# Kernel optimization log

Measured on AMD Instinct MI355X. Metric: run time of the kernel, lower is better.

## Reference

```python
import jax, jax.numpy as jnp
import numpy as np

B, S, H, A, F, NCATE, VOCAB, EMB, NCONT = 64, 1024, 512, 256, 2048, 4, 1000, 64, 4


def _layernorm(x, g, b, eps=1e-5):
    m = jnp.mean(x, axis=-1, keepdims=True)
    v = jnp.mean((x - m) ** 2, axis=-1, keepdims=True)
    return (x - m) * jax.lax.rsqrt(v + eps) * g + b


def _positional_encoding(seq_len, d, base=10000.0):
    pos = jnp.arange(seq_len, dtype=jnp.float32)[:, None]
    i = jnp.arange(0, d, 2, dtype=jnp.float32)[None, :]
    ang = pos / jnp.power(base, i / d)
    pe = jnp.zeros((seq_len, d), dtype=jnp.float32)
    pe = pe.at[:, 0::2].set(jnp.sin(ang))
    pe = pe.at[:, 1::2].set(jnp.cos(ang))
    return pe


def setup_inputs() -> dict:
    key = jax.random.key(0)
    ks = jax.random.split(key, 24)
    s = lambda i, shape, fan: jax.random.normal(ks[i], shape, jnp.float32) / np.sqrt(fan)
    inp = {
        'cate_x': jax.random.randint(ks[0], (B, S, NCATE), 0, VOCAB, jnp.int32),
        'cont_x': jax.random.normal(ks[1], (B, S, NCONT), jnp.float32),
        'mask': (jax.random.uniform(ks[2], (B, S)) < 0.9).astype(jnp.float32),
        'targets': jax.random.uniform(ks[3], (B, S), jnp.float32),
        'E_cate': s(4, (NCATE, VOCAB, EMB), EMB),
        'W_proj': s(5, (NCATE * EMB + NCONT, H), NCATE * EMB + NCONT),
        'WQ1': s(6, (H, A), H), 'WK1': s(7, (H, A), H), 'WV1': s(8, (H, A), H),
        'WQ2': s(9, (H, A), H), 'WK2': s(10, (H, A), H), 'WV2': s(11, (H, A), H),
        'W0': s(12, (2 * A, H), 2 * A),
        'ln1_g': jnp.ones((H,), jnp.float32), 'ln1_b': jnp.zeros((H,), jnp.float32),
        'Wf1': s(13, (H, F), H), 'bf1': jnp.zeros((F,), jnp.float32),
        'Wf2': s(14, (F, H), F), 'bf2': jnp.zeros((H,), jnp.float32),
        'ln2_g': jnp.ones((H,), jnp.float32), 'ln2_b': jnp.zeros((H,), jnp.float32),
        'Wfin': s(15, (H, 1), H), 'bfin': jnp.zeros((1,), jnp.float32),
    }
    return inp


def _attn_branch(x, WQ, WK, WV, mask_bias):
    Q = x @ WQ  # [B,S,A]
    K = x @ WK
    V = x @ WV
    scores = jnp.einsum('bsa,bta->bst', Q, K) / np.sqrt(A)
    scores = scores + mask_bias  # additive key-mask [B,1,S]
    return jnp.einsum('bst,bta->bsa', jax.nn.softmax(scores, axis=-1), V)


def reference(cate_x, cont_x, mask, targets, E_cate, W_proj, WQ1, WK1, WV1,
              WQ2, WK2, WV2, W0, ln1_g, ln1_b, Wf1, bf1, Wf2, bf2, ln2_g,
              ln2_b, Wfin, bfin):
    # embedding: per-feature lookup, concat with continuous, project to hidden
    emb = jax.vmap(lambda tab, idx: tab[idx], in_axes=(0, 2), out_axes=2)(E_cate, cate_x)
    emb = emb.reshape(B, S, NCATE * EMB)
    x = jnp.concatenate([emb, cont_x], axis=-1) @ W_proj  # [B,S,H]
    x = x + _positional_encoding(S, H)[None]
    mask_bias = (mask * 1e6 - 1e6)[:, None, :]  # [B,1,S]
    z1 = _attn_branch(x, WQ1, WK1, WV1, mask_bias)
    z2 = _attn_branch(x, WQ2, WK2, WV2, mask_bias)
    z = jnp.concatenate([z1, z2], axis=-1) @ W0
    z = _layernorm(x + z, ln1_g, ln1_b)
    fz = jax.nn.relu(z @ Wf1 + bf1) @ Wf2 + bf2
    z3 = _layernorm(z + fz, ln2_g, ln2_b)
    out = (z3 @ Wfin + bfin).squeeze(-1)  # [B,S]
    return out
```

## Files before the change

### kernel.cpp

```cpp
#include <hip/hip_runtime.h>

typedef unsigned short ushort_t;
typedef unsigned int uint32;
typedef float f32x4 __attribute__((ext_vector_type(4)));
typedef short bf16x8 __attribute__((ext_vector_type(8)));

__device__ __forceinline__ float bf2f(short u) {
  union { uint32 u32; float f; } cv;
  cv.u32 = ((uint32)(ushort_t)u) << 16;
  return cv.f;
}
__device__ __forceinline__ ushort_t f2bf(float f) {
  union { float f; uint32 u; } cv; cv.f = f;
  return (ushort_t)((cv.u + 0x7fffu + ((cv.u >> 16) & 1u)) >> 16);
}
__device__ __forceinline__ uint32 pack2bf(float lo, float hi) {
  return (uint32)f2bf(lo) | ((uint32)f2bf(hi) << 16);
}
__device__ __forceinline__ f32x4 mfma16(bf16x8 a, bf16x8 b, f32x4 c) {
  return __builtin_amdgcn_mfma_f32_16x16x32_bf16(a, b, c, 0, 0, 0);
}
__device__ __forceinline__ void gld_lds16(const ushort_t* g, ushort_t* l) {
  __builtin_amdgcn_global_load_lds(
      (const __attribute__((address_space(1))) void*)g,
      (__attribute__((address_space(3))) void*)l, 16, 0, 0);
}

__global__ __launch_bounds__(256)
void transpose_w(const float* __restrict__ W, ushort_t* __restrict__ WT, int K, int N) {
  __shared__ float s[32][33];
  const int tx = threadIdx.x & 31, ty = threadIdx.x >> 5;
  const int k0 = blockIdx.x * 32, n0 = blockIdx.y * 32;
#pragma unroll
  for (int i = 0; i < 4; ++i)
    s[ty + i * 8][tx] = W[(size_t)(k0 + ty + i * 8) * N + n0 + tx];
  __syncthreads();
#pragma unroll
  for (int i = 0; i < 4; ++i)
    WT[(size_t)(n0 + ty + i * 8) * K + k0 + tx] = f2bf(s[tx][ty + i * 8]);
}

__global__ __launch_bounds__(256)
void ep_kernel(const float* __restrict__ E, const float* __restrict__ Wp,
               ushort_t* __restrict__ EP) {
  const int cv = blockIdx.x;
  const int c = cv / 1000;
  __shared__ float se[64];
  if (threadIdx.x < 64) se[threadIdx.x] = E[(size_t)cv * 64 + threadIdx.x];
  __syncthreads();
  const float* wrow = Wp + (size_t)c * 64 * 512;
  for (int h = threadIdx.x; h < 512; h += 256) {
    float acc = 0.f;
#pragma unroll
    for (int e = 0; e < 64; ++e) acc += se[e] * wrow[(size_t)e * 512 + h];
    EP[(size_t)cv * 512 + h] = f2bf(acc);
  }
}

__global__ __launch_bounds__(256)
void pe_kernel(float* __restrict__ PE) {
  const int id = blockIdx.x * 256 + threadIdx.x;
  const int s = id >> 8, i = id & 255;
  const float ang = (float)s * exp2f(-(float)i * (13.287712379549449f / 256.0f));
  PE[(size_t)s * 512 + 2 * i] = sinf(ang);
  PE[(size_t)s * 512 + 2 * i + 1] = cosf(ang);
}

__global__ __launch_bounds__(256)
void x_kernel(const int* __restrict__ cate, const float* __restrict__ cont,
              const float* __restrict__ Wp, const ushort_t* __restrict__ EP,
              const float* __restrict__ PE, ushort_t* __restrict__ X) {
  const int tid = threadIdx.x;
  const size_t r = (size_t)blockIdx.x * 4 + (tid >> 6);
  const int lane = tid & 63;
  const int h0 = lane * 8;
  const int s = (int)(r & 1023);
  float acc[8];
  const float4 p0 = *(const float4*)(PE + (size_t)s * 512 + h0);
  const float4 p1 = *(const float4*)(PE + (size_t)s * 512 + h0 + 4);
  acc[0] = p0.x; acc[1] = p0.y; acc[2] = p0.z; acc[3] = p0.w;
  acc[4] = p1.x; acc[5] = p1.y; acc[6] = p1.z; acc[7] = p1.w;
#pragma unroll
  for (int c = 0; c < 4; ++c) {
    const int idx = cate[r * 4 + c];
    const bf16x8 e8 = *(const bf16x8*)(EP + ((size_t)(c * 1000 + idx)) * 512 + h0);
#pragma unroll
    for (int k = 0; k < 8; ++k) acc[k] += bf2f(e8[k]);
  }
#pragma unroll
  for (int j = 0; j < 4; ++j) {
    const float cj = cont[r * 4 + j];
    const float4 w0 = *(const float4*)(Wp + (size_t)(256 + j) * 512 + h0);
    const float4 w1 = *(const float4*)(Wp + (size_t)(256 + j) * 512 + h0 + 4);
    acc[0] += cj * w0.x; acc[1] += cj * w0.y; acc[2] += cj * w0.z; acc[3] += cj * w0.w;
    acc[4] += cj * w1.x; acc[5] += cj * w1.y; acc[6] += cj * w1.z; acc[7] += cj * w1.w;
  }
  bf16x8 ov;
#pragma unroll
  for (int k = 0; k < 8; ++k) ov[k] = (short)f2bf(acc[k]);
  *(bf16x8*)(X + r * 512 + h0) = ov;
}

template <int EPI, bool TSTORE>
__global__ __launch_bounds__(256, 2)
void gemm_bt(const ushort_t* __restrict__ A, const ushort_t* __restrict__ BT,
             ushort_t* __restrict__ C, const float* __restrict__ bias, int N, int K) {
  __shared__ __align__(16) ushort_t sA[128 * 64];
  __shared__ __align__(16) ushort_t sB[128 * 64];
  const int tid = threadIdx.x;
  const int lane = tid & 63;
  const int wid = tid >> 6;
  const int l15 = lane & 15, l4 = lane >> 4;
  const int wr = (wid >> 1) * 64, wc = (wid & 1) * 64;
  const size_t rowA0 = (size_t)blockIdx.x * 128;
  const size_t rowB0 = (size_t)blockIdx.y * 128;

  f32x4 acc[4][4] = {};

  for (int kt = 0; kt < K; kt += 64) {
#pragma unroll
    for (int it = 0; it < 4; ++it) {
      const int L = it * 256 + tid;
      const int row = L >> 3;
      const int c = (L & 7) ^ (row & 7);
      gld_lds16(A + (rowA0 + row) * K + kt + c * 8, sA + (size_t)L * 8);
      gld_lds16(BT + (rowB0 + row) * K + kt + c * 8, sB + (size_t)L * 8);
    }
    __syncthreads();
#pragma unroll
    for (int kk = 0; kk < 2; ++kk) {
      bf16x8 af[4], bfr[4];
#pragma unroll
      for (int mi = 0; mi < 4; ++mi) {
        const int row = wr + mi * 16 + l15;
        const int c = (kk * 4 + l4) ^ (row & 7);
        af[mi] = *(const bf16x8*)(sA + row * 64 + c * 8);
      }
#pragma unroll
      for (int ni = 0; ni < 4; ++ni) {
        const int row = wc + ni * 16 + l15;
        const int c = (kk * 4 + l4) ^ (row & 7);
        bfr[ni] = *(const bf16x8*)(sB + row * 64 + c * 8);
      }
#pragma unroll
      for (int mi = 0; mi < 4; ++mi)
#pragma unroll
        for (int ni = 0; ni < 4; ++ni)
          acc[mi][ni] = mfma16(af[mi], bfr[ni], acc[mi][ni]);
    }
    __syncthreads();
  }
#pragma unroll
  for (int ni = 0; ni < 4; ++ni) {
    const int col = (int)rowB0 + wc + ni * 16 + l15;
    float bv = 0.f;
    if (EPI > 0) bv = bias[col];
#pragma unroll
    for (int mi = 0; mi < 4; ++mi) {
      const size_t row0 = rowA0 + wr + mi * 16 + l4 * 4;
      if (TSTORE) {
        ushort4 ov;
        ov.x = f2bf(acc[mi][ni][0]);
        ov.y = f2bf(acc[mi][ni][1]);
        ov.z = f2bf(acc[mi][ni][2]);
        ov.w = f2bf(acc[mi][ni][3]);
        *(ushort4*)(C + ((row0 >> 10) * 256 + (size_t)col) * 1024 + (row0 & 1023)) = ov;
      } else {
#pragma unroll
        for (int j = 0; j < 4; ++j) {
          float v = acc[mi][ni][j] + bv;
          if (EPI == 2) v = fmaxf(v, 0.f);
          C[(row0 + j) * N + col] = f2bf(v);
        }
      }
    }
  }
}

__global__ __launch_bounds__(256, 2)
void attn_kernel(const ushort_t* __restrict__ Q, const ushort_t* __restrict__ Kb,
                 const ushort_t* __restrict__ VT, const float* __restrict__ mask,
                 ushort_t* __restrict__ Z, int colOff) {
  __shared__ __align__(16) ushort_t sK[64 * 256];
  __shared__ __align__(16) ushort_t sV[256 * 64];
  const int tid = threadIdx.x, lane = tid & 63, w = tid >> 6;
  const int l15 = lane & 15, l4 = lane >> 4;
  const int id = blockIdx.x;
  const int b = ((id >> 7) << 3) | (id & 7);
  const int qb = (id >> 3) & 15;
  const int q0 = qb * 64 + w * 16;

  bf16x8 qf[8];
  {
    const ushort_t* qrow = Q + ((size_t)b * 1024 + q0 + l15) * 256;
#pragma unroll
    for (int kk = 0; kk < 8; ++kk)
      qf[kk] = *(const bf16x8*)(qrow + kk * 32 + l4 * 8);
  }
  float m_run = -3.0e38f, l_run = 0.f;
  f32x4 o[16] = {};
  const int src0 = ((l4 & 1) << 5) + l15;
  const bool hiSel = (l4 >= 2);

  for (int t0 = 0; t0 < 1024; t0 += 64) {
#pragma unroll
    for (int it = 0; it < 8; ++it) {
      const int L = it * 256 + tid;
      const int rk = L >> 5;
      const int ck = (L & 24) | ((L ^ rk) & 7);
      gld_lds16(Kb + ((size_t)b * 1024 + t0 + rk) * 256 + ck * 8, sK + (size_t)L * 8);
      const int rv = L >> 3;
      const int cv2 = (L ^ rv) & 7;
      gld_lds16(VT + ((size_t)b * 256 + rv) * 1024 + t0 + cv2 * 8, sV + (size_t)L * 8);
    }
    __syncthreads();

    f32x4 st[4] = {};
#pragma unroll
    for (int fi = 0; fi < 4; ++fi) {
      const int row = fi * 16 + l15;
      const ushort_t* kr = sK + row * 256;
#pragma unroll
      for (int kk = 0; kk < 8; ++kk) {
        const int c = kk * 4 + l4;
        const int cs = (c & 24) | ((c ^ row) & 7);
        const bf16x8 kf = *(const bf16x8*)(kr + cs * 8);
        st[fi] = mfma16(kf, qf[kk], st[fi]);
      }
    }

    float pr[4][4];
    float tmax = -3.0e38f;
#pragma unroll
    for (int fi = 0; fi < 4; ++fi) {
      const float4 mk = *(const float4*)(mask + (size_t)b * 1024 + t0 + fi * 16 + l4 * 4);
      pr[fi][0] = st[fi][0] * 0.0625f + (mk.x * 1e6f - 1e6f);
      pr[fi][1] = st[fi][1] * 0.0625f + (mk.y * 1e6f - 1e6f);
      pr[fi][2] = st[fi][2] * 0.0625f + (mk.z * 1e6f - 1e6f);
      pr[fi][3] = st[fi][3] * 0.0625f + (mk.w * 1e6f - 1e6f);
      tmax = fmaxf(tmax, fmaxf(fmaxf(pr[fi][0], pr[fi][1]), fmaxf(pr[fi][2], pr[fi][3])));
    }
    tmax = fmaxf(tmax, __shfl_xor(tmax, 16));
    tmax = fmaxf(tmax, __shfl_xor(tmax, 32));

    if (!__all(tmax <= m_run + 8.f)) {
      const float m_new = fmaxf(m_run, tmax);
      const float alpha = __expf(m_run - m_new);
      l_run *= alpha;
      m_run = m_new;
#pragma unroll
      for (int ai = 0; ai < 16; ++ai) o[ai] *= alpha;
    }

    float rs = 0.f;
#pragma unroll
    for (int fi = 0; fi < 4; ++fi)
#pragma unroll
      for (int j = 0; j < 4; ++j) {
        pr[fi][j] = __expf(pr[fi][j] - m_run);
        rs += pr[fi][j];
      }
    rs += __shfl_xor(rs, 16);
    rs += __shfl_xor(rs, 32);
    l_run += rs;

    uint32 pk[4][2];
#pragma unroll
    for (int fi = 0; fi < 4; ++fi) {
      pk[fi][0] = pack2bf(pr[fi][0], pr[fi][1]);
      pk[fi][1] = pack2bf(pr[fi][2], pr[fi][3]);
    }
    bf16x8 pf[2];
#pragma unroll
    for (int kk2 = 0; kk2 < 2; ++kk2) {
      const uint32 a0 = __shfl(pk[2 * kk2][0], src0);
      const uint32 a1 = __shfl(pk[2 * kk2][1], src0);
      const uint32 a2 = __shfl(pk[2 * kk2][0], src0 + 16);
      const uint32 a3 = __shfl(pk[2 * kk2][1], src0 + 16);
      const uint32 b0 = __shfl(pk[2 * kk2 + 1][0], src0);
      const uint32 b1 = __shfl(pk[2 * kk2 + 1][1], src0);
      const uint32 b2 = __shfl(pk[2 * kk2 + 1][0], src0 + 16);
      const uint32 b3 = __shfl(pk[2 * kk2 + 1][1], src0 + 16);
      uint4 wv;
      wv.x = hiSel ? b0 : a0;
      wv.y = hiSel ? b1 : a1;
      wv.z = hiSel ? b2 : a2;
      wv.w = hiSel ? b3 : a3;
      pf[kk2] = __builtin_bit_cast(bf16x8, wv);
    }

#pragma unroll
    for (int ai = 0; ai < 16; ++ai) {
      const int row = ai * 16 + l15;
      const ushort_t* vr = sV + row * 64;
#pragma unroll
      for (int kk2 = 0; kk2 < 2; ++kk2) {
        const int c = (kk2 * 4 + l4) ^ (row & 7);
        const bf16x8 vf = *(const bf16x8*)(vr + c * 8);
        o[ai] = mfma16(vf, pf[kk2], o[ai]);
      }
    }
    __syncthreads();
  }

  const float inv = 1.f / l_run;
  const size_t zrow = ((size_t)b * 1024 + q0 + l15) * 512;
#pragma unroll
  for (int ai = 0; ai < 16; ++ai) {
    ushort4 ov;
    ov.x = f2bf(o[ai][0] * inv);
    ov.y = f2bf(o[ai][1] * inv);
    ov.z = f2bf(o[ai][2] * inv);
    ov.w = f2bf(o[ai][3] * inv);
    *(ushort4*)(Z + zrow + colOff + ai * 16 + l4 * 4) = ov;
  }
}

__global__ __launch_bounds__(256)
void ln_kernel(const ushort_t* __restrict__ Xa, const ushort_t* __restrict__ Xb2,
               const float* __restrict__ g, const float* __restrict__ bb,
               ushort_t* __restrict__ O) {
  const int tid = threadIdx.x;
  const size_t r = (size_t)blockIdx.x * 4 + (tid >> 6);
  const int lane = tid & 63;
  const int h0 = lane * 8;
  const bf16x8 va = *(const bf16x8*)(Xa + r * 512 + h0);
  const bf16x8 vb = *(const bf16x8*)(Xb2 + r * 512 + h0);
  float v[8], s1 = 0.f, s2 = 0.f;
#pragma unroll
  for (int k = 0; k < 8; ++k) {
    v[k] = bf2f(va[k]) + bf2f(vb[k]);
    s1 += v[k];
    s2 += v[k] * v[k];
  }
#pragma unroll
  for (int m = 1; m < 64; m <<= 1) {
    s1 += __shfl_xor(s1, m);
    s2 += __shfl_xor(s2, m);
  }
  const float mean = s1 * (1.f / 512.f);
  const float var = s2 * (1.f / 512.f) - mean * mean;
  const float rstd = rsqrtf(var + 1e-5f);
  const float4 g0 = *(const float4*)(g + h0);
  const float4 g1 = *(const float4*)(g + h0 + 4);
  const float4 b0 = *(const float4*)(bb + h0);
  const float4 b1 = *(const float4*)(bb + h0 + 4);
  const float gg[8] = {g0.x, g0.y, g0.z, g0.w, g1.x, g1.y, g1.z, g1.w};
  const float bbv[8] = {b0.x, b0.y, b0.z, b0.w, b1.x, b1.y, b1.z, b1.w};
  bf16x8 ov;
#pragma unroll
  for (int k = 0; k < 8; ++k)
    ov[k] = (short)f2bf((v[k] - mean) * rstd * gg[k] + bbv[k]);
  *(bf16x8*)(O + r * 512 + h0) = ov;
}

__global__ __launch_bounds__(256)
void ln_fin_kernel(const ushort_t* __restrict__ Xa, const ushort_t* __restrict__ Xb2,
                   const float* __restrict__ g, const float* __restrict__ bb,
                   const float* __restrict__ Wfin, const float* __restrict__ bfin,
                   float* __restrict__ out) {
  const int tid = threadIdx.x;
  const size_t r = (size_t)blockIdx.x * 4 + (tid >> 6);
  const int lane = tid & 63;
  const int h0 = lane * 8;
  const bf16x8 va = *(const bf16x8*)(Xa + r * 512 + h0);
  const bf16x8 vb = *(const bf16x8*)(Xb2 + r * 512 + h0);
  float v[8], s1 = 0.f, s2 = 0.f;
#pragma unroll
  for (int k = 0; k < 8; ++k) {
    v[k] = bf2f(va[k]) + bf2f(vb[k]);
    s1 += v[k];
    s2 += v[k] * v[k];
  }
#pragma unroll
  for (int m = 1; m < 64; m <<= 1) {
    s1 += __shfl_xor(s1, m);
    s2 += __shfl_xor(s2, m);
  }
  const float mean = s1 * (1.f / 512.f);
  const float var = s2 * (1.f / 512.f) - mean * mean;
  const float rstd = rsqrtf(var + 1e-5f);
  const float4 g0 = *(const float4*)(g + h0);
  const float4 g1 = *(const float4*)(g + h0 + 4);
  const float4 b0 = *(const float4*)(bb + h0);
  const float4 b1 = *(const float4*)(bb + h0 + 4);
  const float4 w0 = *(const float4*)(Wfin + h0);
  const float4 w1 = *(const float4*)(Wfin + h0 + 4);
  const float gg[8] = {g0.x, g0.y, g0.z, g0.w, g1.x, g1.y, g1.z, g1.w};
  const float bbv[8] = {b0.x, b0.y, b0.z, b0.w, b1.x, b1.y, b1.z, b1.w};
  const float ww[8] = {w0.x, w0.y, w0.z, w0.w, w1.x, w1.y, w1.z, w1.w};
  float dot = 0.f;
#pragma unroll
  for (int k = 0; k < 8; ++k)
    dot += ((v[k] - mean) * rstd * gg[k] + bbv[k]) * ww[k];
#pragma unroll
  for (int m = 1; m < 64; m <<= 1) dot += __shfl_xor(dot, m);
  if (lane == 0) out[r] = dot + bfin[0];
}

extern "C" void kernel_launch(void* const* d_in, const int* in_sizes, int n_in,
                              void* d_out, int out_size, void* d_ws, size_t ws_size,
                              hipStream_t stream) {
  (void)in_sizes; (void)n_in; (void)out_size; (void)ws_size;
  const int* cate   = (const int*)d_in[0];
  const float* cont = (const float*)d_in[1];
  const float* mask = (const float*)d_in[2];
  const float* E    = (const float*)d_in[4];
  const float* Wp   = (const float*)d_in[5];
  const float* WQ1  = (const float*)d_in[6];
  const float* WK1  = (const float*)d_in[7];
  const float* WV1  = (const float*)d_in[8];
  const float* WQ2  = (const float*)d_in[9];
  const float* WK2  = (const float*)d_in[10];
  const float* WV2  = (const float*)d_in[11];
  const float* W0   = (const float*)d_in[12];
  const float* ln1g = (const float*)d_in[13];
  const float* ln1b = (const float*)d_in[14];
  const float* Wf1  = (const float*)d_in[15];
  const float* bf1  = (const float*)d_in[16];
  const float* Wf2  = (const float*)d_in[17];
  const float* bf2  = (const float*)d_in[18];
  const float* ln2g = (const float*)d_in[19];
  const float* ln2b = (const float*)d_in[20];
  const float* Wfin = (const float*)d_in[21];
  const float* bfin = (const float*)d_in[22];
  float* out = (float*)d_out;
  char* ws = (char*)d_ws;

  const size_t MB = 1ull << 20;
  ushort_t* Xb  = (ushort_t*)(ws + 0);
  ushort_t* Qb  = (ushort_t*)(ws + 64 * MB);
  ushort_t* Kb  = (ushort_t*)(ws + 96 * MB);
  ushort_t* VTb = (ushort_t*)(ws + 128 * MB);
  ushort_t* Zb  = (ushort_t*)(ws + 160 * MB);
  ushort_t* T0b = (ushort_t*)(ws + 64 * MB);
  ushort_t* H1b = (ushort_t*)(ws + 128 * MB);
  ushort_t* Gb  = (ushort_t*)(ws + 0);
  ushort_t* T1b = (ushort_t*)(ws + 64 * MB);
  const size_t OW = 224 * MB;
  ushort_t* wq1t = (ushort_t*)(ws + OW + 0);
  ushort_t* wk1t = (ushort_t*)(ws + OW + 262144);
  ushort_t* wv1t = (ushort_t*)(ws + OW + 524288);
  ushort_t* wq2t = (ushort_t*)(ws + OW + 786432);
  ushort_t* wk2t = (ushort_t*)(ws + OW + 1048576);
  ushort_t* wv2t = (ushort_t*)(ws + OW + 1310720);
  ushort_t* w0t  = (ushort_t*)(ws + OW + 1572864);
  ushort_t* wf1t = (ushort_t*)(ws + OW + 2097152);
  ushort_t* wf2t = (ushort_t*)(ws + OW + 4194304);
  ushort_t* epb  = (ushort_t*)(ws + OW + 6291456);
  float*    peb  = (float*)   (ws + OW + 10485760);

  const dim3 blk(256);
  transpose_w<<<dim3(16, 8), blk, 0, stream>>>(WQ1, wq1t, 512, 256);
  transpose_w<<<dim3(16, 8), blk, 0, stream>>>(WK1, wk1t, 512, 256);
  transpose_w<<<dim3(16, 8), blk, 0, stream>>>(WV1, wv1t, 512, 256);
  transpose_w<<<dim3(16, 8), blk, 0, stream>>>(WQ2, wq2t, 512, 256);
  transpose_w<<<dim3(16, 8), blk, 0, stream>>>(WK2, wk2t, 512, 256);
  transpose_w<<<dim3(16, 8), blk, 0, stream>>>(WV2, wv2t, 512, 256);
  transpose_w<<<dim3(16, 16), blk, 0, stream>>>(W0, w0t, 512, 512);
  transpose_w<<<dim3(16, 64), blk, 0, stream>>>(Wf1, wf1t, 512, 2048);
  transpose_w<<<dim3(64, 16), blk, 0, stream>>>(Wf2, wf2t, 2048, 512);
  ep_kernel<<<4000, blk, 0, stream>>>(E, Wp, epb);
  pe_kernel<<<1024, blk, 0, stream>>>(peb);
  x_kernel<<<16384, blk, 0, stream>>>(cate, cont, Wp, epb, peb, Xb);
  gemm_bt<0, false><<<dim3(512, 2), blk, 0, stream>>>(Xb, wq1t, Qb, nullptr, 256, 512);
  gemm_bt<0, false><<<dim3(512, 2), blk, 0, stream>>>(Xb, wk1t, Kb, nullptr, 256, 512);
  gemm_bt<0, true><<<dim3(512, 2), blk, 0, stream>>>(Xb, wv1t, VTb, nullptr, 256, 512);
  attn_kernel<<<dim3(1024), blk, 0, stream>>>(Qb, Kb, VTb, mask, Zb, 0);
  gemm_bt<0, false><<<dim3(512, 2), blk, 0, stream>>>(Xb, wq2t, Qb, nullptr, 256, 512);
  gemm_bt<0, false><<<dim3(512, 2), blk, 0, stream>>>(Xb, wk2t, Kb, nullptr, 256, 512);
  gemm_bt<0, true><<<dim3(512, 2), blk, 0, stream>>>(Xb, wv2t, VTb, nullptr, 256, 512);
  attn_kernel<<<dim3(1024), blk, 0, stream>>>(Qb, Kb, VTb, mask, Zb, 256);
  gemm_bt<0, false><<<dim3(512, 4), blk, 0, stream>>>(Zb, w0t, T0b, nullptr, 512, 512);
  ln_kernel<<<16384, blk, 0, stream>>>(Xb, T0b, ln1g, ln1b, H1b);
  for (int rc = 0; rc < 4; ++rc) {
    const ushort_t* h1c = H1b + (size_t)rc * 16384 * 512;
    ushort_t* t1c = T1b + (size_t)rc * 16384 * 512;
    gemm_bt<2, false><<<dim3(128, 16), blk, 0, stream>>>(h1c, wf1t, Gb, bf1, 2048, 512);
    gemm_bt<1, false><<<dim3(128, 4), blk, 0, stream>>>(Gb, wf2t, t1c, bf2, 512, 2048);
  }
  ln_fin_kernel<<<16384, blk, 0, stream>>>(H1b, T1b, ln2g, ln2b, Wfin, bfin, out);
}
```

Measured before the change: 1.009 ms.

## Switch attention kernel to 32x32x16 MFMA with 128-query blocks

```diff
diff --git a/kernel.cpp b/kernel.cpp
--- a/kernel.cpp
+++ b/kernel.cpp
@@ -3,6 +3,7 @@
 typedef unsigned short ushort_t;
 typedef unsigned int uint32;
 typedef float f32x4 __attribute__((ext_vector_type(4)));
+typedef float f32x16 __attribute__((ext_vector_type(16)));
 typedef short bf16x8 __attribute__((ext_vector_type(8)));
 
 __device__ __forceinline__ float bf2f(short u) {
@@ -19,6 +20,9 @@
 }
 __device__ __forceinline__ f32x4 mfma16(bf16x8 a, bf16x8 b, f32x4 c) {
   return __builtin_amdgcn_mfma_f32_16x16x32_bf16(a, b, c, 0, 0, 0);
+}
+__device__ __forceinline__ f32x16 mfma32(bf16x8 a, bf16x8 b, f32x16 c) {
+  return __builtin_amdgcn_mfma_f32_32x32x16_bf16(a, b, c, 0, 0, 0);
 }
 __device__ __forceinline__ void gld_lds16(const ushort_t* g, ushort_t* l) {
   __builtin_amdgcn_global_load_lds(
@@ -184,23 +188,21 @@
   __shared__ __align__(16) ushort_t sK[64 * 256];
   __shared__ __align__(16) ushort_t sV[256 * 64];
   const int tid = threadIdx.x, lane = tid & 63, w = tid >> 6;
-  const int l15 = lane & 15, l4 = lane >> 4;
+  const int l31 = lane & 31, hi = lane >> 5;
   const int id = blockIdx.x;
-  const int b = ((id >> 7) << 3) | (id & 7);
-  const int qb = (id >> 3) & 15;
-  const int q0 = qb * 64 + w * 16;
-
-  bf16x8 qf[8];
+  const int b = ((id >> 6) << 3) | (id & 7);
+  const int qb = (id >> 3) & 7;
+  const int q0 = qb * 128 + w * 32;
+
+  bf16x8 qf[16];
   {
-    const ushort_t* qrow = Q + ((size_t)b * 1024 + q0 + l15) * 256;
-#pragma unroll
-    for (int kk = 0; kk < 8; ++kk)
-      qf[kk] = *(const bf16x8*)(qrow + kk * 32 + l4 * 8);
+    const ushort_t* qrow = Q + ((size_t)b * 1024 + q0 + l31) * 256 + hi * 8;
+#pragma unroll
+    for (int kc = 0; kc < 16; ++kc)
+      qf[kc] = *(const bf16x8*)(qrow + kc * 16);
   }
   float m_run = -3.0e38f, l_run = 0.f;
-  f32x4 o[16] = {};
-  const int src0 = ((l4 & 1) << 5) + l15;
-  const bool hiSel = (l4 >= 2);
+  f32x16 o[8] = {};
 
   for (int t0 = 0; t0 < 1024; t0 += 64) {
 #pragma unroll
@@ -215,32 +217,34 @@
     }
     __syncthreads();
 
-    f32x4 st[4] = {};
-#pragma unroll
-    for (int fi = 0; fi < 4; ++fi) {
-      const int row = fi * 16 + l15;
-      const ushort_t* kr = sK + row * 256;
-#pragma unroll
-      for (int kk = 0; kk < 8; ++kk) {
-        const int c = kk * 4 + l4;
+    f32x16 st[2] = {};
+#pragma unroll
+    for (int ts = 0; ts < 2; ++ts) {
+      const int row = ts * 32 + l31;
+      const ushort_t* krow = sK + row * 256;
+#pragma unroll
+      for (int kc = 0; kc < 16; ++kc) {
+        const int c = kc * 2 + hi;
         const int cs = (c & 24) | ((c ^ row) & 7);
-        const bf16x8 kf = *(const bf16x8*)(kr + cs * 8);
-        st[fi] = mfma16(kf, qf[kk], st[fi]);
-      }
-    }
-
-    float pr[4][4];
+        const bf16x8 kf = *(const bf16x8*)(krow + cs * 8);
+        st[ts] = mfma32(kf, qf[kc], st[ts]);
+      }
+    }
+
     float tmax = -3.0e38f;
 #pragma unroll
-    for (int fi = 0; fi < 4; ++fi) {
-      const float4 mk = *(const float4*)(mask + (size_t)b * 1024 + t0 + fi * 16 + l4 * 4);
-      pr[fi][0] = st[fi][0] * 0.0625f + (mk.x * 1e6f - 1e6f);
-      pr[fi][1] = st[fi][1] * 0.0625f + (mk.y * 1e6f - 1e6f);
-      pr[fi][2] = st[fi][2] * 0.0625f + (mk.z * 1e6f - 1e6f);
-      pr[fi][3] = st[fi][3] * 0.0625f + (mk.w * 1e6f - 1e6f);
-      tmax = fmaxf(tmax, fmaxf(fmaxf(pr[fi][0], pr[fi][1]), fmaxf(pr[fi][2], pr[fi][3])));
-    }
-    tmax = fmaxf(tmax, __shfl_xor(tmax, 16));
+    for (int ts = 0; ts < 2; ++ts)
+#pragma unroll
+      for (int g = 0; g < 4; ++g) {
+        const float4 mk =
+            *(const float4*)(mask + (size_t)b * 1024 + t0 + ts * 32 + g * 8 + hi * 4);
+        st[ts][4 * g + 0] = st[ts][4 * g + 0] * 0.0625f + (mk.x * 1e6f - 1e6f);
+        st[ts][4 * g + 1] = st[ts][4 * g + 1] * 0.0625f + (mk.y * 1e6f - 1e6f);
+        st[ts][4 * g + 2] = st[ts][4 * g + 2] * 0.0625f + (mk.z * 1e6f - 1e6f);
+        st[ts][4 * g + 3] = st[ts][4 * g + 3] * 0.0625f + (mk.w * 1e6f - 1e6f);
+        tmax = fmaxf(tmax, fmaxf(fmaxf(st[ts][4 * g + 0], st[ts][4 * g + 1]),
+                                 fmaxf(st[ts][4 * g + 2], st[ts][4 * g + 3])));
+      }
     tmax = fmaxf(tmax, __shfl_xor(tmax, 32));
 
     if (!__all(tmax <= m_run + 8.f)) {
@@ -249,71 +253,69 @@
       l_run *= alpha;
       m_run = m_new;
 #pragma unroll
-      for (int ai = 0; ai < 16; ++ai) o[ai] *= alpha;
+      for (int at = 0; at < 8; ++at) o[at] *= alpha;
     }
 
     float rs = 0.f;
-#pragma unroll
-    for (int fi = 0; fi < 4; ++fi)
-#pragma unroll
-      for (int j = 0; j < 4; ++j) {
-        pr[fi][j] = __expf(pr[fi][j] - m_run);
-        rs += pr[fi][j];
-      }
-    rs += __shfl_xor(rs, 16);
+    bf16x8 pf[2][2];
+#pragma unroll
+    for (int ts = 0; ts < 2; ++ts)
+#pragma unroll
+      for (int kc = 0; kc < 2; ++kc) {
+        float e[8];
+#pragma unroll
+        for (int j = 0; j < 8; ++j) {
+          e[j] = __expf(st[ts][kc * 8 + j] - m_run);
+          rs += e[j];
+        }
+        const uint32 wl0 = pack2bf(e[0], e[1]);
+        const uint32 wl1 = pack2bf(e[2], e[3]);
+        const uint32 wh0 = pack2bf(e[4], e[5]);
+        const uint32 wh1 = pack2bf(e[6], e[7]);
+        const uint32 sl0 = __shfl_xor(wl0, 32);
+        const uint32 sl1 = __shfl_xor(wl1, 32);
+        const uint32 sh0 = __shfl_xor(wh0, 32);
+        const uint32 sh1 = __shfl_xor(wh1, 32);
+        uint4 u;
+        u.x = hi ? sh0 : wl0;
+        u.y = hi ? sh1 : wl1;
+        u.z = hi ? wh0 : sl0;
+        u.w = hi ? wh1 : sl1;
+        pf[ts][kc] = __builtin_bit_cast(bf16x8, u);
+      }
     rs += __shfl_xor(rs, 32);
     l_run += rs;
 
-    uint32 pk[4][2];
-#pragma unroll
-    for (int fi = 0; fi < 4; ++fi) {
-      pk[fi][0] = pack2bf(pr[fi][0], pr[fi][1]);
-      pk[fi][1] = pack2bf(pr[fi][2], pr[fi][3]);
-    }
-    bf16x8 pf[2];
-#pragma unroll
-    for (int kk2 = 0; kk2 < 2; ++kk2) {
-      const uint32 a0 = __shfl(pk[2 * kk2][0], src0);
-      const uint32 a1 = __shfl(pk[2 * kk2][1], src0);
-      const uint32 a2 = __shfl(pk[2 * kk2][0], src0 + 16);
-      const uint32 a3 = __shfl(pk[2 * kk2][1], src0 + 16);
-      const uint32 b0 = __shfl(pk[2 * kk2 + 1][0], src0);
-      const uint32 b1 = __shfl(pk[2 * kk2 + 1][1], src0);
-      const uint32 b2 = __shfl(pk[2 * kk2 + 1][0], src0 + 16);
-      const uint32 b3 = __shfl(pk[2 * kk2 + 1][1], src0 + 16);
-      uint4 wv;
-      wv.x = hiSel ? b0 : a0;
-      wv.y = hiSel ? b1 : a1;
-      wv.z = hiSel ? b2 : a2;
-      wv.w = hiSel ? b3 : a3;
-      pf[kk2] = __builtin_bit_cast(bf16x8, wv);
-    }
-
-#pragma unroll
-    for (int ai = 0; ai < 16; ++ai) {
-      const int row = ai * 16 + l15;
-      const ushort_t* vr = sV + row * 64;
-#pragma unroll
-      for (int kk2 = 0; kk2 < 2; ++kk2) {
-        const int c = (kk2 * 4 + l4) ^ (row & 7);
-        const bf16x8 vf = *(const bf16x8*)(vr + c * 8);
-        o[ai] = mfma16(vf, pf[kk2], o[ai]);
-      }
+#pragma unroll
+    for (int at = 0; at < 8; ++at) {
+      const int row = at * 32 + l31;
+      const ushort_t* vrow = sV + row * 64;
+#pragma unroll
+      for (int ts = 0; ts < 2; ++ts)
+#pragma unroll
+        for (int kc = 0; kc < 2; ++kc) {
+          const int c = ts * 4 + kc * 2 + hi;
+          const int cs = (c ^ row) & 7;
+          const bf16x8 vf = *(const bf16x8*)(vrow + cs * 8);
+          o[at] = mfma32(vf, pf[ts][kc], o[at]);
+        }
     }
     __syncthreads();
   }
 
   const float inv = 1.f / l_run;
-  const size_t zrow = ((size_t)b * 1024 + q0 + l15) * 512;
-#pragma unroll
-  for (int ai = 0; ai < 16; ++ai) {
-    ushort4 ov;
-    ov.x = f2bf(o[ai][0] * inv);
-    ov.y = f2bf(o[ai][1] * inv);
-    ov.z = f2bf(o[ai][2] * inv);
-    ov.w = f2bf(o[ai][3] * inv);
-    *(ushort4*)(Z + zrow + colOff + ai * 16 + l4 * 4) = ov;
-  }
+  ushort_t* zbase = Z + ((size_t)b * 1024 + q0 + l31) * 512 + colOff;
+#pragma unroll
+  for (int at = 0; at < 8; ++at)
+#pragma unroll
+    for (int g = 0; g < 4; ++g) {
+      ushort4 ov;
+      ov.x = f2bf(o[at][4 * g + 0] * inv);
+      ov.y = f2bf(o[at][4 * g + 1] * inv);
+      ov.z = f2bf(o[at][4 * g + 2] * inv);
+      ov.w = f2bf(o[at][4 * g + 3] * inv);
+      *(ushort4*)(zbase + at * 32 + g * 8 + hi * 4) = ov;
+    }
 }
 
 __global__ __launch_bounds__(256)
@@ -466,11 +468,11 @@
   gemm_bt<0, false><<<dim3(512, 2), blk, 0, stream>>>(Xb, wq1t, Qb, nullptr, 256, 512);
   gemm_bt<0, false><<<dim3(512, 2), blk, 0, stream>>>(Xb, wk1t, Kb, nullptr, 256, 512);
   gemm_bt<0, true><<<dim3(512, 2), blk, 0, stream>>>(Xb, wv1t, VTb, nullptr, 256, 512);
-  attn_kernel<<<dim3(1024), blk, 0, stream>>>(Qb, Kb, VTb, mask, Zb, 0);
+  attn_kernel<<<dim3(512), blk, 0, stream>>>(Qb, Kb, VTb, mask, Zb, 0);
   gemm_bt<0, false><<<dim3(512, 2), blk, 0, stream>>>(Xb, wq2t, Qb, nullptr, 256, 512);
   gemm_bt<0, false><<<dim3(512, 2), blk, 0, stream>>>(Xb, wk2t, Kb, nullptr, 256, 512);
   gemm_bt<0, true><<<dim3(512, 2), blk, 0, stream>>>(Xb, wv2t, VTb, nullptr, 256, 512);
-  attn_kernel<<<dim3(1024), blk, 0, stream>>>(Qb, Kb, VTb, mask, Zb, 256);
+  attn_kernel<<<dim3(512), blk, 0, stream>>>(Qb, Kb, VTb, mask, Zb, 256);
   gemm_bt<0, false><<<dim3(512, 4), blk, 0, stream>>>(Zb, w0t, T0b, nullptr, 512, 512);
   ln_kernel<<<16384, blk, 0, stream>>>(Xb, T0b, ln1g, ln1b, H1b);
   for (int rc = 0; rc < 4; ++rc) {
```

New measurement: 1.184 ms. +17.3%, slower.

## Add 256-row, 512-thread triple-buffered GEMM for the FFN layers

Applied to the files above, without the earlier changes.

```diff
diff --git a/kernel.cpp b/kernel.cpp
--- a/kernel.cpp
+++ b/kernel.cpp
@@ -172,6 +172,104 @@
           if (EPI == 2) v = fmaxf(v, 0.f);
           C[(row0 + j) * N + col] = f2bf(v);
         }
+      }
+    }
+  }
+}
+
+template <int EPI, int BN>
+__global__ __launch_bounds__(512, 2)
+void gemm256(const ushort_t* __restrict__ A, const ushort_t* __restrict__ BT,
+             ushort_t* __restrict__ C, const float* __restrict__ bias, int N, int K) {
+  constexpr int ATILE = 256 * 32;
+  constexpr int BTILE = BN * 32;
+  constexpr int WN = BN / 4;
+  constexpr int NREP = WN / 16;
+  __shared__ __align__(16) ushort_t sA[3][ATILE];
+  __shared__ __align__(16) ushort_t sB[3][BTILE];
+  const int tid = threadIdx.x;
+  const int lane = tid & 63;
+  const int wid = tid >> 6;
+  const int l15 = lane & 15, l4 = lane >> 4;
+  const int wm = wid >> 2, wn = wid & 3;
+  const size_t rowA0 = (size_t)blockIdx.x * 256;
+  const size_t rowB0 = (size_t)blockIdx.y * BN;
+
+  f32x4 acc[8][NREP] = {};
+
+  auto stage = [&](int buf, int kt) {
+#pragma unroll
+    for (int j = 0; j < 2; ++j) {
+      const int L = j * 512 + tid;
+      const int row = L >> 2;
+      const int c = (L & 3) ^ (row & 3);
+      gld_lds16(A + (rowA0 + row) * K + kt + c * 8, sA[buf] + (size_t)L * 8);
+    }
+#pragma unroll
+    for (int j = 0; j < BN / 128; ++j) {
+      const int L = j * 512 + tid;
+      const int row = L >> 2;
+      const int c = (L & 3) ^ (row & 3);
+      gld_lds16(BT + (rowB0 + row) * K + kt + c * 8, sB[buf] + (size_t)L * 8);
+    }
+  };
+  auto compute = [&](int buf) {
+    bf16x8 af[8], bfr[NREP];
+#pragma unroll
+    for (int mi = 0; mi < 8; ++mi) {
+      const int row = wm * 128 + mi * 16 + l15;
+      const int cs = l4 ^ (row & 3);
+      af[mi] = *(const bf16x8*)(sA[buf] + row * 32 + cs * 8);
+    }
+#pragma unroll
+    for (int ni = 0; ni < NREP; ++ni) {
+      const int row = wn * WN + ni * 16 + l15;
+      const int cs = l4 ^ (row & 3);
+      bfr[ni] = *(const bf16x8*)(sB[buf] + row * 32 + cs * 8);
+    }
+#pragma unroll
+    for (int mi = 0; mi < 8; ++mi)
+#pragma unroll
+      for (int ni = 0; ni < NREP; ++ni)
+        acc[mi][ni] = mfma16(af[mi], bfr[ni], acc[mi][ni]);
+  };
+
+  const int NT = K >> 5;
+  stage(0, 0);
+  stage(1, 32);
+  int buf = 0;
+  for (int i = 0; i < NT; ++i) {
+    if (i < NT - 1) {
+      if constexpr (BN == 256)
+        asm volatile("s_waitcnt vmcnt(4)" ::: "memory");
+      else
+        asm volatile("s_waitcnt vmcnt(3)" ::: "memory");
+    } else {
+      asm volatile("s_waitcnt vmcnt(0)" ::: "memory");
+    }
+    __builtin_amdgcn_sched_barrier(0);
+    __builtin_amdgcn_s_barrier();
+    __builtin_amdgcn_sched_barrier(0);
+    if (i + 2 < NT) {
+      int nb = buf + 2; if (nb >= 3) nb -= 3;
+      stage(nb, (i + 2) * 32);
+    }
+    compute(buf);
+    if (++buf == 3) buf = 0;
+  }
+
+#pragma unroll
+  for (int ni = 0; ni < NREP; ++ni) {
+    const int col = (int)rowB0 + wn * WN + ni * 16 + l15;
+    const float bv = bias[col];
+#pragma unroll
+    for (int mi = 0; mi < 8; ++mi) {
+      const size_t row0 = rowA0 + wm * 128 + mi * 16 + l4 * 4;
+#pragma unroll
+      for (int j = 0; j < 4; ++j) {
+        float v = acc[mi][ni][j] + bv;
+        if (EPI == 2) v = fmaxf(v, 0.f);
+        C[(row0 + j) * N + col] = f2bf(v);
       }
     }
   }
@@ -476,8 +574,8 @@
   for (int rc = 0; rc < 4; ++rc) {
     const ushort_t* h1c = H1b + (size_t)rc * 16384 * 512;
     ushort_t* t1c = T1b + (size_t)rc * 16384 * 512;
-    gemm_bt<2, false><<<dim3(128, 16), blk, 0, stream>>>(h1c, wf1t, Gb, bf1, 2048, 512);
-    gemm_bt<1, false><<<dim3(128, 4), blk, 0, stream>>>(Gb, wf2t, t1c, bf2, 512, 2048);
+    gemm256<2, 256><<<dim3(64, 8), dim3(512), 0, stream>>>(h1c, wf1t, Gb, bf1, 2048, 512);
+    gemm256<1, 128><<<dim3(64, 4), dim3(512), 0, stream>>>(Gb, wf2t, t1c, bf2, 512, 2048);
   }
   ln_fin_kernel<<<16384, blk, 0, stream>>>(H1b, T1b, ln2g, ln2b, Wfin, bfin, out);
 }
```

New measurement: 1.190 ms. 1.18x slower.
